# Performance work log

Measured on AMD Instinct MI355X. Metric: run time of the kernel, lower is better.

Reference implementation:

```python
import jax, jax.numpy as jnp
import numpy as np

ALPHA = 0.25
GAMMA = 2.0
MARGIN = 1.0
LAMBDA_GRAPH = 0.1
N = 8192
D = 128


def setup_inputs() -> dict:
    key = jax.random.key(0)
    k1, k2, k3, k4 = jax.random.split(key, 4)
    preds = jax.random.normal(k1, (N,), dtype=jnp.float32)
    targets = jax.random.randint(k2, (N,), 0, 2).astype(jnp.float32)  # binary labels
    features = jax.random.normal(k3, (N, D), dtype=jnp.float32)
    graph_features = jax.random.normal(k4, (N, D), dtype=jnp.float32)
    return {"preds": preds, "targets": targets, "features": features,
            "graph_features": graph_features}


def _focal_loss(preds, targets):
    # numerically stable BCE-with-logits, reduction='none'
    bce = jnp.maximum(preds, 0.0) - preds * targets + jnp.log1p(jnp.exp(-jnp.abs(preds)))
    pt = jnp.exp(-bce)
    return jnp.mean(ALPHA * (1.0 - pt) ** GAMMA * bce)


def _contrastive_loss(features, labels):
    # squared pairwise distances via ||a||^2 + ||b||^2 - 2 a.b  -> [N, N]
    sqn = jnp.sum(features * features, axis=-1)
    sq = sqn[:, None] + sqn[None, :] - 2.0 * (features @ features.T)
    sq = jnp.maximum(sq, 0.0)
    # safe sqrt (gradient-safe at 0)
    pos = sq > 0.0
    dist = jnp.where(pos, jnp.sqrt(jnp.where(pos, sq, 1.0)), 0.0)
    same = labels[:, None] == labels[None, :]
    # same-label pairs: dist^2 == sq ; different: clamp(margin - dist, 0)^2
    per_pair = jnp.where(same, sq, jnp.maximum(MARGIN - dist, 0.0) ** 2)
    return jnp.mean(per_pair)  # sum / N^2


def _graph_reg_loss(graph_features):
    diff = graph_features[1:] - graph_features[:-1]
    return jnp.mean(jnp.sqrt(jnp.sum(diff * diff, axis=1)))


def reference(preds, targets, features, graph_features):
    return (_focal_loss(preds, targets)
            + _contrastive_loss(features, targets)
            + LAMBDA_GRAPH * _graph_reg_loss(graph_features))
```

## Files before the change

### kernel.cpp

```cpp
#include <hip/hip_runtime.h>
#include <hip/hip_bf16.h>


#define N_PTS 8192
#define DIM 128

typedef __bf16 bf16x8 __attribute__((ext_vector_type(8)));
typedef float f32x4 __attribute__((ext_vector_type(4)));

#define FBF_OFF   0
#define SQN_OFF   (N_PTS * DIM * 2)
#define CPART_OFF (SQN_OFF + N_PTS * 4)
#define FPART_OFF (CPART_OFF + 8320 * 4)
#define GPART_OFF (FPART_OFF + 32 * 4)
#define VPART_OFF (GPART_OFF + 256 * 4)

__global__ __launch_bounds__(256) void aux_kernel(const float* __restrict__ feat,
                                                  const float* __restrict__ preds,
                                                  const float* __restrict__ targets,
                                                  const float* __restrict__ gfeat,
                                                  __bf16* __restrict__ fbf,
                                                  float* __restrict__ sqn,
                                                  float* __restrict__ vpart,
                                                  float* __restrict__ f_part,
                                                  float* __restrict__ g_part) {
    __shared__ __align__(16) char smem[8192];
    const int bx = blockIdx.x;
    const int tid = threadIdx.x;
    const int w = tid >> 6;
    const int lane = tid & 63;

    if (bx < 512) {
        const int g = bx;
        const float4* feat4 = reinterpret_cast<const float4*>(feat);
        const float4 a = feat4[g * 512 + tid * 2];
        const float4 b = feat4[g * 512 + tid * 2 + 1];
        const int m = tid >> 4, c = tid & 15;
        union { __bf16 h[8]; uint4 u; } pk;
        pk.h[0] = (__bf16)a.x; pk.h[1] = (__bf16)a.y;
        pk.h[2] = (__bf16)a.z; pk.h[3] = (__bf16)a.w;
        pk.h[4] = (__bf16)b.x; pk.h[5] = (__bf16)b.y;
        pk.h[6] = (__bf16)b.z; pk.h[7] = (__bf16)b.w;
        *reinterpret_cast<uint4*>(smem + c * 256 + m * 16) = pk.u;
        float s = a.x * a.x + a.y * a.y + a.z * a.z + a.w * a.w
                + b.x * b.x + b.y * b.y + b.z * b.z + b.w * b.w;
        s += __shfl_down(s, 8); s += __shfl_down(s, 4);
        s += __shfl_down(s, 2); s += __shfl_down(s, 1);
        if (c == 0) sqn[g * 16 + m] = s;
        __syncthreads();
        reinterpret_cast<uint4*>(fbf)[g * 256 + tid] =
            *reinterpret_cast<const uint4*>(smem + tid * 16);
    } else if (bx < 544) {
        const int b = bx - 512;
        const float2* feat2 = reinterpret_cast<const float2*>(feat);
        float2 accA = {0.f, 0.f}, acc1 = {0.f, 0.f};
        int r = b * 256 + w * 64;
        #pragma unroll 4
        for (int i = 0; i < 64; ++i, ++r) {
            const float2 v = feat2[r * 64 + lane];
            const float tr = targets[r];
            accA.x += v.x; accA.y += v.y;
            acc1.x += tr * v.x; acc1.y += tr * v.y;
        }
        float* fA = reinterpret_cast<float*>(smem);
        float* f1 = reinterpret_cast<float*>(smem + 2048);
        fA[w * 128 + 2 * lane] = accA.x; fA[w * 128 + 2 * lane + 1] = accA.y;
        f1[w * 128 + 2 * lane] = acc1.x; f1[w * 128 + 2 * lane + 1] = acc1.y;
        __syncthreads();
        if (tid < 128) {
            const int d = tid;
            const float c1 = f1[d] + f1[128 + d] + f1[256 + d] + f1[384 + d];
            const float ca = fA[d] + fA[128 + d] + fA[256 + d] + fA[384 + d];
            vpart[b * 256 + tid] = ca - c1;
        } else {
            const int d = tid - 128;
            vpart[b * 256 + tid] = f1[d] + f1[128 + d] + f1[256 + d] + f1[384 + d];
        }
    } else if (bx < 576) {
        const int b = bx - 544;
        const int i = b * 256 + tid;
        const float p = preds[i], t = targets[i];
        const float bce = fmaxf(p, 0.f) - p * t + log1pf(expf(-fabsf(p)));
        const float pt = expf(-bce);
        const float om = 1.f - pt;
        float v = 0.25f * om * om * bce;
        #pragma unroll
        for (int off = 32; off > 0; off >>= 1) v += __shfl_down(v, off);
        float* red = reinterpret_cast<float*>(smem);
        if (lane == 0) red[w] = v;
        __syncthreads();
        if (tid == 0) f_part[b] = red[0] + red[1] + red[2] + red[3];
    } else {
        const int b = bx - 576;
        float acc = 0.f;
        #pragma unroll
        for (int it = 0; it < 8; ++it) {
            const int r = b * 4 + w + it * 1024;
            if (r < N_PTS - 1) {
                const float2 a = *reinterpret_cast<const float2*>(gfeat + r * DIM + lane * 2);
                const float2 bb = *reinterpret_cast<const float2*>(gfeat + (r + 1) * DIM + lane * 2);
                const float dx = bb.x - a.x, dy = bb.y - a.y;
                float s = dx * dx + dy * dy;
                #pragma unroll
                for (int off = 32; off > 0; off >>= 1) s += __shfl_down(s, off);
                if (lane == 0) acc += sqrtf(s);
            }
        }
        float* red = reinterpret_cast<float*>(smem);
        if (lane == 0) red[w] = acc;
        __syncthreads();
        if (tid == 0) g_part[b] = red[0] + red[1] + red[2] + red[3];
    }
}

template<bool DIAG>
__device__ __forceinline__ float scan_slow(const f32x4 (&acc)[4][4],
                                           const f32x4 (&sqni)[4], const f32x4 (&ti4)[4],
                                           const float (&sqnj)[4], const float (&tj4)[4],
                                           int wm, int wn, int quad, int m15) {
    float lsum = 0.f;
    #pragma unroll
    for (int tm = 0; tm < 4; ++tm) {
        #pragma unroll
        for (int tn = 0; tn < 4; ++tn) {
            const int jl = wn * 64 + tn * 16 + m15;
            #pragma unroll
            for (int e = 0; e < 4; ++e) {
                const float sq = sqni[tm][e] + sqnj[tn] - 2.f * acc[tm][tn][e];
                bool excl = (ti4[tm][e] == tj4[tn]);
                if (DIAG) {
                    const int il = wm * 64 + tm * 16 + quad * 4 + e;
                    excl = excl || (jl <= il);
                }
                if (!excl && sq < 1.f) {
                    const float d = sqrtf(fmaxf(sq, 0.f));
                    const float m = 1.f - d;
                    lsum += 2.f * m * m;
                }
            }
        }
    }
    return lsum;
}

__global__ __launch_bounds__(256) void pair_kernel(const __bf16* __restrict__ fbf,
                                                   const float* __restrict__ sqn,
                                                   const float* __restrict__ targets,
                                                   float* __restrict__ c_part) {
    const int u = blockIdx.x;
    const int v = 2079 - u;
    int k = (int)((sqrtf(8.f * (float)v + 1.f) - 1.f) * 0.5f);
    while ((k + 1) * (k + 2) / 2 <= v) ++k;
    while (k * (k + 1) / 2 > v) --k;
    const int bi = 63 - k;
    const int bj = 63 - (v - k * (k + 1) / 2);

    const int tid = threadIdx.x;
    const int lane = tid & 63;
    const int wv = tid >> 6;
    const int quad = lane >> 4;
    const int m15 = lane & 15;
    const int wm = wv >> 1, wn = wv & 1;
    const int ibase = bi * 128, jbase = bj * 128;

    const uint4* fp = reinterpret_cast<const uint4*>(fbf);
    const uint4* base_a = fp + (bi * 8 + wm * 4) * 256 + quad * 16 + m15;
    const uint4* base_b = fp + (bj * 8 + wn * 4) * 256 + quad * 16 + m15;
    bf16x8 af[4][4], bfr[4][4];
    #pragma unroll
    for (int t = 0; t < 4; ++t)
        #pragma unroll
        for (int ks = 0; ks < 4; ++ks) {
            af[t][ks]  = *reinterpret_cast<const bf16x8*>(base_a + t * 256 + ks * 64);
            bfr[t][ks] = *reinterpret_cast<const bf16x8*>(base_b + t * 256 + ks * 64);
        }

    f32x4 acc[4][4];
    #pragma unroll
    for (int a = 0; a < 4; ++a)
        #pragma unroll
        for (int b = 0; b < 4; ++b) acc[a][b] = (f32x4){0.f, 0.f, 0.f, 0.f};

    #pragma unroll
    for (int ks = 0; ks < 4; ++ks)
        #pragma unroll
        for (int tm = 0; tm < 4; ++tm)
            #pragma unroll
            for (int tn = 0; tn < 4; ++tn)
                acc[tm][tn] = __builtin_amdgcn_mfma_f32_16x16x32_bf16(
                    af[tm][ks], bfr[tn][ks], acc[tm][tn], 0, 0, 0);

    f32x4 sqni[4], ti4[4];
    float sqnj[4], tj4[4];
    #pragma unroll
    for (int tm = 0; tm < 4; ++tm) {
        const int i0 = wm * 64 + tm * 16 + quad * 4;
        sqni[tm] = *reinterpret_cast<const f32x4*>(sqn + ibase + i0);
        ti4[tm]  = *reinterpret_cast<const f32x4*>(targets + ibase + i0);
    }
    #pragma unroll
    for (int tn = 0; tn < 4; ++tn) {
        const int jl = wn * 64 + tn * 16 + m15;
        sqnj[tn] = sqn[jbase + jl];
        tj4[tn]  = targets[jbase + jl];
    }

    float minkey = 1e30f;
    #pragma unroll
    for (int tm = 0; tm < 4; ++tm)
        #pragma unroll
        for (int tn = 0; tn < 4; ++tn)
            #pragma unroll
            for (int e = 0; e < 4; ++e) {
                const float sq = fmaf(-2.f, acc[tm][tn][e], sqni[tm][e]) + sqnj[tn];
                minkey = fminf(minkey, sq);
            }

    const bool diag = (bi == bj);
    float lsum = 0.f;
    if (minkey < 2.f)
        lsum = diag
            ? scan_slow<true >(acc, sqni, ti4, sqnj, tj4, wm, wn, quad, m15)
            : scan_slow<false>(acc, sqni, ti4, sqnj, tj4, wm, wn, quad, m15);

    #pragma unroll
    for (int off = 32; off > 0; off >>= 1) lsum += __shfl_down(lsum, off);
    if (lane == 0) c_part[u * 4 + wv] = lsum;
}

__global__ __launch_bounds__(256) void finalize_kernel(const float* __restrict__ c_part,
                                                       const float* __restrict__ f_part,
                                                       const float* __restrict__ g_part,
                                                       const float* __restrict__ vpart,
                                                       const float* __restrict__ sqn,
                                                       const float* __restrict__ targets,
                                                       float* __restrict__ out) {
    __shared__ float red[32];
    const int tid = threadIdx.x;
    const int w = tid >> 6, lane = tid & 63;

    float c = 0.f;
    for (int i = tid; i < 8320; i += 256) c += c_part[i];
    float f = (tid < 32) ? f_part[tid] : 0.f;
    float g = g_part[tid];

    float V = 0.f;
    #pragma unroll 8
    for (int b = 0; b < 32; ++b) V += vpart[b * 256 + tid];
    float vsq = V * V;

    float stot = 0.f, s1 = 0.f, n1 = 0.f;
    for (int i = tid; i < N_PTS; i += 256) {
        const float s = sqn[i], t = targets[i];
        stot += s; s1 += t * s; n1 += t;
    }

    #pragma unroll
    for (int off = 32; off > 0; off >>= 1) {
        c += __shfl_down(c, off);
        f += __shfl_down(f, off);
        g += __shfl_down(g, off);
        vsq  += __shfl_down(vsq, off);
        stot += __shfl_down(stot, off);
        s1   += __shfl_down(s1, off);
        n1   += __shfl_down(n1, off);
    }
    if (lane == 0) {
        red[w] = c; red[4 + w] = f; red[8 + w] = g;
        red[12 + w] = vsq; red[16 + w] = stot; red[20 + w] = s1; red[24 + w] = n1;
    }
    __syncthreads();
    if (tid == 0) {
        const double cs = (double)red[0] + red[1] + red[2] + red[3];
        const double fs = (double)red[4] + red[5] + red[6] + red[7];
        const double gs = (double)red[8] + red[9] + red[10] + red[11];
        const double v0sq = (double)red[12] + red[13];
        const double v1sq = (double)red[14] + red[15];
        const double st = (double)red[16] + red[17] + red[18] + red[19];
        const double s1s = (double)red[20] + red[21] + red[22] + red[23];
        const double n1s = (double)red[24] + red[25] + red[26] + red[27];
        const double n0s = (double)N_PTS - n1s;
        const double s0s = st - s1s;
        const double same = 2.0 * (n0s * s0s - v0sq) + 2.0 * (n1s * s1s - v1sq);
        out[0] = (float)((cs + same) / ((double)N_PTS * N_PTS)
                         + fs / N_PTS + 0.1 * (gs / (N_PTS - 1)));
    }
}

extern "C" void kernel_launch(void* const* d_in, const int* in_sizes, int n_in,
                              void* d_out, int out_size, void* d_ws, size_t ws_size,
                              hipStream_t stream) {
    const float* preds    = (const float*)d_in[0];
    const float* targets  = (const float*)d_in[1];
    const float* features = (const float*)d_in[2];
    const float* gfeat    = (const float*)d_in[3];
    char* ws = (char*)d_ws;
    __bf16* fbf   = (__bf16*)(ws + FBF_OFF);
    float* sqn    = (float*)(ws + SQN_OFF);
    float* c_part = (float*)(ws + CPART_OFF);
    float* f_part = (float*)(ws + FPART_OFF);
    float* g_part = (float*)(ws + GPART_OFF);
    float* vpart  = (float*)(ws + VPART_OFF);
    float* out = (float*)d_out;

    aux_kernel<<<832, 256, 0, stream>>>(features, preds, targets, gfeat,
                                        fbf, sqn, vpart, f_part, g_part);
    pair_kernel<<<2080, 256, 0, stream>>>(fbf, sqn, targets, c_part);
    finalize_kernel<<<1, 256, 0, stream>>>(c_part, f_part, g_part, vpart, sqn, targets, out);
}
```

Baseline: 111.7 us.

## Screen pair tiles with a cheap one-step MFMA distance bound before the full GEMM

```diff
diff --git a/kernel.cpp b/kernel.cpp
--- a/kernel.cpp
+++ b/kernel.cpp
@@ -9,17 +9,21 @@
 typedef float f32x4 __attribute__((ext_vector_type(4)));
 
 #define FBF_OFF   0
-#define SQN_OFF   (N_PTS * DIM * 2)
-#define CPART_OFF (SQN_OFF + N_PTS * 4)
-#define FPART_OFF (CPART_OFF + 8320 * 4)
-#define GPART_OFF (FPART_OFF + 32 * 4)
-#define VPART_OFF (GPART_OFF + 256 * 4)
+#define SQN_OFF   2097152
+#define CPART_OFF 2129920
+#define FPART_OFF 2163200
+#define GPART_OFF 2163328
+#define VPART_OFF 2164352
+#define ASCR_OFF  2197120
+#define BSCR_OFF  2721408
 
 __global__ __launch_bounds__(256) void aux_kernel(const float* __restrict__ feat,
                                                   const float* __restrict__ preds,
                                                   const float* __restrict__ targets,
                                                   const float* __restrict__ gfeat,
                                                   __bf16* __restrict__ fbf,
+                                                  __bf16* __restrict__ ascr,
+                                                  __bf16* __restrict__ bscr,
                                                   float* __restrict__ sqn,
                                                   float* __restrict__ vpart,
                                                   float* __restrict__ f_part,
@@ -42,14 +46,46 @@
         pk.h[4] = (__bf16)b.x; pk.h[5] = (__bf16)b.y;
         pk.h[6] = (__bf16)b.z; pk.h[7] = (__bf16)b.w;
         *reinterpret_cast<uint4*>(smem + c * 256 + m * 16) = pk.u;
-        float s = a.x * a.x + a.y * a.y + a.z * a.z + a.w * a.w
-                + b.x * b.x + b.y * b.y + b.z * b.z + b.w * b.w;
-        s += __shfl_down(s, 8); s += __shfl_down(s, 4);
-        s += __shfl_down(s, 2); s += __shfl_down(s, 1);
-        if (c == 0) sqn[g * 16 + m] = s;
+        if (c < 3) {
+            union { __bf16 h[8]; uint4 u; } pa;
+            pa.h[0] = (__bf16)(-2.f * a.x); pa.h[1] = (__bf16)(-2.f * a.y);
+            pa.h[2] = (__bf16)(-2.f * a.z); pa.h[3] = (__bf16)(-2.f * a.w);
+            pa.h[4] = (__bf16)(-2.f * b.x); pa.h[5] = (__bf16)(-2.f * b.y);
+            pa.h[6] = (__bf16)(-2.f * b.z); pa.h[7] = (__bf16)(-2.f * b.w);
+            *reinterpret_cast<uint4*>(smem + 4096 + c * 256 + m * 16) = pa.u;
+            *reinterpret_cast<uint4*>(smem + 5120 + c * 256 + m * 16) = pk.u;
+        }
+        const float s = a.x * a.x + a.y * a.y + a.z * a.z + a.w * a.w
+                      + b.x * b.x + b.y * b.y + b.z * b.z + b.w * b.w;
+        reinterpret_cast<float*>(smem + 6144)[m * 16 + c] = s;
+        __syncthreads();
+        if (c == 3) {
+            const float* S = reinterpret_cast<const float*>(smem + 6144);
+            const float sq24 = S[m * 16] + S[m * 16 + 1] + S[m * 16 + 2];
+            union { __bf16 h[8]; uint4 u; } pa, pb;
+            #pragma unroll
+            for (int k = 0; k < 8; ++k) { pa.h[k] = (__bf16)0.f; pb.h[k] = (__bf16)0.f; }
+            pa.h[0] = (__bf16)sq24; pa.h[1] = (__bf16)1.f;
+            pb.h[0] = (__bf16)1.f;  pb.h[1] = (__bf16)sq24;
+            *reinterpret_cast<uint4*>(smem + 4096 + 3 * 256 + m * 16) = pa.u;
+            *reinterpret_cast<uint4*>(smem + 5120 + 3 * 256 + m * 16) = pb.u;
+        }
+        if (c == 0) {
+            const float* S = reinterpret_cast<const float*>(smem + 6144);
+            float t = 0.f;
+            #pragma unroll
+            for (int k = 0; k < 16; ++k) t += S[m * 16 + k];
+            sqn[g * 16 + m] = t;
+        }
         __syncthreads();
         reinterpret_cast<uint4*>(fbf)[g * 256 + tid] =
             *reinterpret_cast<const uint4*>(smem + tid * 16);
+        if (tid < 64)
+            reinterpret_cast<uint4*>(ascr)[g * 64 + tid] =
+                *reinterpret_cast<const uint4*>(smem + 4096 + tid * 16);
+        else if (tid < 128)
+            reinterpret_cast<uint4*>(bscr)[g * 64 + (tid - 64)] =
+                *reinterpret_cast<const uint4*>(smem + 5120 + (tid - 64) * 16);
     } else if (bx < 544) {
         const int b = bx - 512;
         const float2* feat2 = reinterpret_cast<const float2*>(feat);
@@ -143,10 +179,12 @@
     return lsum;
 }
 
-__global__ __launch_bounds__(256) void pair_kernel(const __bf16* __restrict__ fbf,
-                                                   const float* __restrict__ sqn,
-                                                   const float* __restrict__ targets,
-                                                   float* __restrict__ c_part) {
+__global__ __launch_bounds__(256, 4) void pair_kernel(const __bf16* __restrict__ fbf,
+                                                      const __bf16* __restrict__ ascr,
+                                                      const __bf16* __restrict__ bscr,
+                                                      const float* __restrict__ sqn,
+                                                      const float* __restrict__ targets,
+                                                      float* __restrict__ c_part) {
     const int u = blockIdx.x;
     const int v = 2079 - u;
     int k = (int)((sqrtf(8.f * (float)v + 1.f) - 1.f) * 0.5f);
@@ -163,68 +201,80 @@
     const int wm = wv >> 1, wn = wv & 1;
     const int ibase = bi * 128, jbase = bj * 128;
 
-    const uint4* fp = reinterpret_cast<const uint4*>(fbf);
-    const uint4* base_a = fp + (bi * 8 + wm * 4) * 256 + quad * 16 + m15;
-    const uint4* base_b = fp + (bj * 8 + wn * 4) * 256 + quad * 16 + m15;
-    bf16x8 af[4][4], bfr[4][4];
-    #pragma unroll
-    for (int t = 0; t < 4; ++t)
+    const uint4* aS = reinterpret_cast<const uint4*>(ascr);
+    const uint4* bS = reinterpret_cast<const uint4*>(bscr);
+    const int gA = bi * 8 + wm * 4, gB = bj * 8 + wn * 4;
+    bf16x8 afs[4], bfs[4];
+    #pragma unroll
+    for (int t = 0; t < 4; ++t) {
+        afs[t] = *reinterpret_cast<const bf16x8*>(aS + (gA + t) * 64 + quad * 16 + m15);
+        bfs[t] = *reinterpret_cast<const bf16x8*>(bS + (gB + t) * 64 + quad * 16 + m15);
+    }
+    f32x4 acc[4][4];
+    #pragma unroll
+    for (int a = 0; a < 4; ++a)
+        #pragma unroll
+        for (int b = 0; b < 4; ++b) acc[a][b] = (f32x4){0.f, 0.f, 0.f, 0.f};
+    #pragma unroll
+    for (int tm = 0; tm < 4; ++tm)
+        #pragma unroll
+        for (int tn = 0; tn < 4; ++tn)
+            acc[tm][tn] = __builtin_amdgcn_mfma_f32_16x16x32_bf16(
+                afs[tm], bfs[tn], acc[tm][tn], 0, 0, 0);
+
+    float minl = 1e30f;
+    #pragma unroll
+    for (int tm = 0; tm < 4; ++tm)
+        #pragma unroll
+        for (int tn = 0; tn < 4; ++tn)
+            #pragma unroll
+            for (int e = 0; e < 4; ++e)
+                minl = fminf(minl, acc[tm][tn][e]);
+
+    float lsum = 0.f;
+    if (__any(minl < 2.f)) {
+        f32x4 sqni[4], ti4[4];
+        float sqnj[4], tj4[4];
+        #pragma unroll
+        for (int tm = 0; tm < 4; ++tm) {
+            const int i0 = wm * 64 + tm * 16 + quad * 4;
+            sqni[tm] = *reinterpret_cast<const f32x4*>(sqn + ibase + i0);
+            ti4[tm]  = *reinterpret_cast<const f32x4*>(targets + ibase + i0);
+        }
+        #pragma unroll
+        for (int tn = 0; tn < 4; ++tn) {
+            const int jl = wn * 64 + tn * 16 + m15;
+            sqnj[tn] = sqn[jbase + jl];
+            tj4[tn]  = targets[jbase + jl];
+        }
+        #pragma unroll
+        for (int a = 0; a < 4; ++a)
+            #pragma unroll
+            for (int b = 0; b < 4; ++b) acc[a][b] = (f32x4){0.f, 0.f, 0.f, 0.f};
+        const uint4* fp = reinterpret_cast<const uint4*>(fbf);
+        const uint4* base_a = fp + (bi * 8 + wm * 4) * 256 + quad * 16 + m15;
+        const uint4* base_b = fp + (bj * 8 + wn * 4) * 256 + quad * 16 + m15;
         #pragma unroll
         for (int ks = 0; ks < 4; ++ks) {
-            af[t][ks]  = *reinterpret_cast<const bf16x8*>(base_a + t * 256 + ks * 64);
-            bfr[t][ks] = *reinterpret_cast<const bf16x8*>(base_b + t * 256 + ks * 64);
-        }
-
-    f32x4 acc[4][4];
-    #pragma unroll
-    for (int a = 0; a < 4; ++a)
-        #pragma unroll
-        for (int b = 0; b < 4; ++b) acc[a][b] = (f32x4){0.f, 0.f, 0.f, 0.f};
-
-    #pragma unroll
-    for (int ks = 0; ks < 4; ++ks)
-        #pragma unroll
-        for (int tm = 0; tm < 4; ++tm)
-            #pragma unroll
-            for (int tn = 0; tn < 4; ++tn)
-                acc[tm][tn] = __builtin_amdgcn_mfma_f32_16x16x32_bf16(
-                    af[tm][ks], bfr[tn][ks], acc[tm][tn], 0, 0, 0);
-
-    f32x4 sqni[4], ti4[4];
-    float sqnj[4], tj4[4];
-    #pragma unroll
-    for (int tm = 0; tm < 4; ++tm) {
-        const int i0 = wm * 64 + tm * 16 + quad * 4;
-        sqni[tm] = *reinterpret_cast<const f32x4*>(sqn + ibase + i0);
-        ti4[tm]  = *reinterpret_cast<const f32x4*>(targets + ibase + i0);
-    }
-    #pragma unroll
-    for (int tn = 0; tn < 4; ++tn) {
-        const int jl = wn * 64 + tn * 16 + m15;
-        sqnj[tn] = sqn[jbase + jl];
-        tj4[tn]  = targets[jbase + jl];
-    }
-
-    float minkey = 1e30f;
-    #pragma unroll
-    for (int tm = 0; tm < 4; ++tm)
-        #pragma unroll
-        for (int tn = 0; tn < 4; ++tn)
-            #pragma unroll
-            for (int e = 0; e < 4; ++e) {
-                const float sq = fmaf(-2.f, acc[tm][tn][e], sqni[tm][e]) + sqnj[tn];
-                minkey = fminf(minkey, sq);
+            bf16x8 af[4], bfr[4];
+            #pragma unroll
+            for (int t = 0; t < 4; ++t) {
+                af[t]  = *reinterpret_cast<const bf16x8*>(base_a + t * 256 + ks * 64);
+                bfr[t] = *reinterpret_cast<const bf16x8*>(base_b + t * 256 + ks * 64);
             }
-
-    const bool diag = (bi == bj);
-    float lsum = 0.f;
-    if (minkey < 2.f)
-        lsum = diag
+            #pragma unroll
+            for (int tm = 0; tm < 4; ++tm)
+                #pragma unroll
+                for (int tn = 0; tn < 4; ++tn)
+                    acc[tm][tn] = __builtin_amdgcn_mfma_f32_16x16x32_bf16(
+                        af[tm], bfr[tn], acc[tm][tn], 0, 0, 0);
+        }
+        lsum = (bi == bj)
             ? scan_slow<true >(acc, sqni, ti4, sqnj, tj4, wm, wn, quad, m15)
             : scan_slow<false>(acc, sqni, ti4, sqnj, tj4, wm, wn, quad, m15);
-
-    #pragma unroll
-    for (int off = 32; off > 0; off >>= 1) lsum += __shfl_down(lsum, off);
+        #pragma unroll
+        for (int off = 32; off > 0; off >>= 1) lsum += __shfl_down(lsum, off);
+    }
     if (lane == 0) c_part[u * 4 + wv] = lsum;
 }
 
@@ -296,6 +346,8 @@
     const float* gfeat    = (const float*)d_in[3];
     char* ws = (char*)d_ws;
     __bf16* fbf   = (__bf16*)(ws + FBF_OFF);
+    __bf16* ascr  = (__bf16*)(ws + ASCR_OFF);
+    __bf16* bscr  = (__bf16*)(ws + BSCR_OFF);
     float* sqn    = (float*)(ws + SQN_OFF);
     float* c_part = (float*)(ws + CPART_OFF);
     float* f_part = (float*)(ws + FPART_OFF);
@@ -304,7 +356,7 @@
     float* out = (float*)d_out;
 
     aux_kernel<<<832, 256, 0, stream>>>(features, preds, targets, gfeat,
-                                        fbf, sqn, vpart, f_part, g_part);
-    pair_kernel<<<2080, 256, 0, stream>>>(fbf, sqn, targets, c_part);
+                                        fbf, ascr, bscr, sqn, vpart, f_part, g_part);
+    pair_kernel<<<2080, 256, 0, stream>>>(fbf, ascr, bscr, sqn, targets, c_part);
     finalize_kernel<<<1, 256, 0, stream>>>(c_part, f_part, g_part, vpart, sqn, targets, out);
 }
```

Result: faster. 102.9 us (-7.9%).
